# Optimization experiments

Measured on AMD Instinct MI355X. Metric: run time of the kernel, lower is better.

## Reference

```python
import jax, jax.numpy as jnp
import numpy as np

N = 50000      # nodes
E = 800000     # edges (no self loops; module re-adds them)
F_IN = 128     # feats_per_node
H1, C1 = 8, 32     # conv1: heads=8, out=32 -> concat hidden = 256
H2, C2 = 1, 128    # conv2: heads=1, out=128, concat=False (mean)
NEG = 0.2      # leaky relu slope


def _glorot(key, shape):
    fan_in, fan_out = shape[-1], int(np.prod(shape[:-1]))
    lim = float(np.sqrt(6.0 / (fan_in + fan_out)))
    return jax.random.uniform(key, shape, jnp.float32, -lim, lim)


def setup_inputs() -> dict:
    key = jax.random.key(0)
    ks = jax.random.split(key, 10)
    x = jax.random.normal(ks[0], (N, F_IN), jnp.float32)
    src = jax.random.randint(ks[1], (E,), 0, N, dtype=jnp.int32)
    off = jax.random.randint(ks[2], (E,), 1, N, dtype=jnp.int32)
    dst = (src + off) % N  # guarantees src != dst (no self loops)
    edge_index = jnp.stack([src, dst])  # [2, E], row0=source j, row1=target i
    return {
        "x": x,
        "edge_index": edge_index,
        "lin1_w": _glorot(ks[3], (H1 * C1, F_IN)),
        "att1_i": _glorot(ks[4], (1, H1, C1)),
        "att1_j": _glorot(ks[5], (1, H1, C1)),
        "bias1": jnp.zeros((H1 * C1,), jnp.float32),
        "lin2_w": _glorot(ks[6], (C2, H1 * C1)),
        "att2_i": _glorot(ks[7], (1, H2, C2)),
        "att2_j": _glorot(ks[8], (1, H2, C2)),
        "bias2": jnp.zeros((C2,), jnp.float32),
    }


def _gat_conv(x, src, dst, lin_w, att_i, att_j, bias, heads, out_ch, concat):
    n = x.shape[0]
    xh = (x @ lin_w.T).reshape(n, heads, out_ch)          # [n, H, C]
    # add self loops (input edges have none; module removes then adds)
    sl = jnp.arange(n, dtype=src.dtype)
    s = jnp.concatenate([src, sl])
    d = jnp.concatenate([dst, sl])
    # per-node attention logits, then gather per edge (avoids per-edge dot)
    ai = jnp.sum(xh * att_i, axis=-1)                     # [n, H]
    aj = jnp.sum(xh * att_j, axis=-1)                     # [n, H]
    alpha = ai[d] + aj[s]                                 # [Etot, H]
    alpha = jnp.where(alpha > 0, alpha, NEG * alpha)      # leaky relu
    # segment softmax over destination node (every node has a self loop)
    m = jax.ops.segment_max(alpha, d, num_segments=n)
    alpha = jnp.exp(alpha - m[d])
    denom = jax.ops.segment_sum(alpha, d, num_segments=n)
    alpha = alpha / (denom[d] + 1e-16)
    # weighted scatter-add aggregation
    out = jax.ops.segment_sum(xh[s] * alpha[:, :, None], d, num_segments=n)
    out = out.reshape(n, heads * out_ch) if concat else out.mean(axis=1)
    return out + bias


def reference(x, edge_index, lin1_w, att1_i, att1_j, bias1,
              lin2_w, att2_i, att2_j, bias2):
    src, dst = edge_index[0], edge_index[1]
    h = _gat_conv(x, src, dst, lin1_w, att1_i, att1_j, bias1, H1, C1, True)
    h = jax.nn.elu(h)
    return _gat_conv(h, src, dst, lin2_w, att2_i, att2_j, bias2, H2, C2, False)
```

## Files before the change

kernel.cpp:

```cpp
#include <hip/hip_runtime.h>
#include <math.h>

#define NN   50000
#define NE   800000
#define FIN  128
#define HID  256
#define NH1  8
#define C2   128
#define CAP  64
#define NEGS 0.2f

#define NGRP 196
#define CAPB 4608
#define NBIN 782

#define W1R  272
#define W2R  144

#define SWZ(n) ((((n) & 7)) ^ (((n) >> 4) & 7))

typedef __attribute__((ext_vector_type(8))) short bf16x8;
typedef __attribute__((ext_vector_type(4))) float f32x4;

__device__ inline unsigned short f2bf(float f) {
    union { float f; unsigned u; } v; v.f = f;
    unsigned u = v.u;
    u += 0x7fffu + ((u >> 16) & 1u);
    return (unsigned short)(u >> 16);
}
__device__ inline float bf2f(unsigned short h) {
    union { unsigned u; float f; } v; v.u = ((unsigned)h) << 16;
    return v.f;
}

__global__ __launch_bounds__(256) void k_bin(const int* __restrict__ ei,
                                             int* __restrict__ gcnt,
                                             int* __restrict__ gbuf,
                                             const float* __restrict__ w1,
                                             const float* __restrict__ w2,
                                             const float* __restrict__ a1i,
                                             const float* __restrict__ a1j,
                                             const float* __restrict__ a2i,
                                             const float* __restrict__ a2j,
                                             unsigned short* __restrict__ w1e,
                                             unsigned short* __restrict__ w2e) {
    const int B = blockIdx.x, t = threadIdx.x;
    if (B < NBIN) {
        __shared__ int hcnt[NGRP], hbase[NGRP], h2[NGRP];
        for (int k = t; k < NGRP; k += 256) { hcnt[k] = 0; h2[k] = 0; }
        __syncthreads();
        int sv[4], bv[4];
#pragma unroll
        for (int u = 0; u < 4; ++u) {
            const int e = B * 1024 + u * 256 + t;
            if (e < NE) {
                const int s = ei[e], d = ei[NE + e];
                sv[u] = s | ((d & 255) << 16);
                bv[u] = d >> 8;
                atomicAdd(&hcnt[bv[u]], 1);
            } else bv[u] = -1;
        }
        __syncthreads();
        for (int k = t; k < NGRP; k += 256)
            if (hcnt[k]) hbase[k] = atomicAdd(&gcnt[k], hcnt[k]);
        __syncthreads();
#pragma unroll
        for (int u = 0; u < 4; ++u) {
            if (bv[u] >= 0) {
                const int lp = atomicAdd(&h2[bv[u]], 1);
                const int pos = hbase[bv[u]] + lp;
                if (pos < CAPB) gbuf[(size_t)bv[u] * CAPB + pos] = sv[u];
            }
        }
    } else if (B < 1038) {
        const int g = (B - NBIN) * 256 + t;
        if (g < 32768) w1e[g] = f2bf(w1[g]);
        else w2e[g - 32768] = f2bf(w2[g - 32768]);
    } else if (B < 1046) {
        const int g = (B - 1038) * 256 + t;
        const int r = g >> 7, k = g & 127;
        const int h = r & 7;
        const float* att = (r < 8) ? a1i : a1j;
        float s = 0.f;
        for (int c = 0; c < 32; ++c)
            s += att[h * 32 + c] * w1[(h * 32 + c) * FIN + k];
        w1e[(256 + r) * FIN + k] = f2bf(s);
    } else if (B < 1048) {
        const int g = (B - 1046) * 256 + t;
        const int r = g >> 8, k = g & 255;
        const float* att = (r == 0) ? a2i : a2j;
        float s = 0.f;
        for (int c = 0; c < C2; ++c)
            s += att[c] * w2[c * HID + k];
        w2e[(128 + r) * HID + k] = f2bf(s);
    } else {
        const int g = (B - 1048) * 256 + t;
        w2e[130 * HID + g] = 0;
    }
}

__global__ __launch_bounds__(256) void k_build(const int* __restrict__ gcnt,
                                               const int* __restrict__ gbuf,
                                               int* __restrict__ cnt,
                                               int* __restrict__ csr) {
    const int g = blockIdx.x, t = threadIdx.x;
    __shared__ int ccnt[256];
    ccnt[t] = 0;
    __syncthreads();
    const int n = min(gcnt[g], CAPB);
    const int64_t base = (int64_t)g * CAPB;
    for (int k0 = 0; k0 < n; k0 += 1024) {
        int vv[4];
#pragma unroll
        for (int u = 0; u < 4; ++u) {
            const int k = k0 + u * 256 + t;
            vv[u] = (k < n) ? gbuf[base + k] : -1;
        }
#pragma unroll
        for (int u = 0; u < 4; ++u) {
            if (vv[u] >= 0) {
                const int s = vv[u] & 0xffff;
                const int dlow = (vv[u] >> 16) & 0xff;
                const int slot = atomicAdd(&ccnt[dlow], 1);
                if (slot < CAP)
                    csr[((size_t)g * 256 + dlow) * CAP + slot] = s;
            }
        }
    }
    __syncthreads();
    const int node = g * 256 + t;
    if (node < NN) cnt[node] = ccnt[t];
}

__global__ __launch_bounds__(512, 4) void k_gemm1(const float* __restrict__ x,
                                                  const unsigned short* __restrict__ wb,
                                                  unsigned short* __restrict__ xh,
                                                  unsigned char* __restrict__ xq,
                                                  float* __restrict__ scl,
                                                  float* __restrict__ ai,
                                                  float* __restrict__ aj) {
    __shared__ unsigned short wl[W1R * FIN];
    const int t = threadIdx.x;
    for (int idx = t; idx < W1R * 16; idx += 512) {
        const int row = idx >> 4, c = idx & 15;
        *(int4*)((char*)wl + row * 256 + ((c ^ SWZ(row)) << 4)) =
            *(const int4*)(wb + row * FIN + c * 8);
    }
    __syncthreads();

    const int w = t >> 6, l = t & 63, m = l & 15, q = l >> 4;
    const int arow = blockIdx.x * 128 + w * 16 + m;
    const int rowc = arow < NN ? arow : NN - 1;

    f32x4 acc[17];
#pragma unroll
    for (int nt = 0; nt < 17; ++nt)
#pragma unroll
        for (int b = 0; b < 4; ++b) acc[nt][b] = 0.f;

#pragma unroll
    for (int ks = 0; ks < 4; ++ks) {
        const int k0 = ks * 32 + q * 8;
        const float4 a0 = *(const float4*)(x + (size_t)rowc * FIN + k0);
        const float4 a1 = *(const float4*)(x + (size_t)rowc * FIN + k0 + 4);
        bf16x8 af;
        af[0] = (short)f2bf(a0.x); af[1] = (short)f2bf(a0.y);
        af[2] = (short)f2bf(a0.z); af[3] = (short)f2bf(a0.w);
        af[4] = (short)f2bf(a1.x); af[5] = (short)f2bf(a1.y);
        af[6] = (short)f2bf(a1.z); af[7] = (short)f2bf(a1.w);
        const int cb = ks * 4 + q;
#pragma unroll
        for (int nt = 0; nt < 17; ++nt) {
            const int n = (nt < 16) ? (m * 16 + nt) : (256 + m);
            const bf16x8 bf = *(const bf16x8*)((const char*)wl + n * 256 + ((cb ^ SWZ(n)) << 4));
            acc[nt] = __builtin_amdgcn_mfma_f32_16x16x32_bf16(af, bf, acc[nt], 0, 0, 0);
        }
    }

    const int orow = blockIdx.x * 128 + w * 16 + 4 * q;
#pragma unroll
    for (int b = 0; b < 4; ++b) {
        if (orow + b >= NN) break;
        const int row = orow + b;
        float mx = 1e-20f;
#pragma unroll
        for (int nt = 0; nt < 16; ++nt) mx = fmaxf(mx, fabsf(acc[nt][b]));
#pragma unroll
        for (int off = 1; off < 16; off <<= 1) mx = fmaxf(mx, __shfl_xor(mx, off, 16));
        const float qsc = 127.f / mx;
        unsigned bw[8];
#pragma unroll
        for (int k = 0; k < 8; ++k)
            bw[k] = (unsigned)f2bf(acc[2 * k][b]) | ((unsigned)f2bf(acc[2 * k + 1][b]) << 16);
        int4* bd = (int4*)(xh + (size_t)row * HID + m * 16);
        bd[0] = make_int4(bw[0], bw[1], bw[2], bw[3]);
        bd[1] = make_int4(bw[4], bw[5], bw[6], bw[7]);
        unsigned qw[4];
#pragma unroll
        for (int k = 0; k < 4; ++k) {
            const int q0 = (int)rintf(acc[4 * k + 0][b] * qsc) + 128;
            const int q1 = (int)rintf(acc[4 * k + 1][b] * qsc) + 128;
            const int q2 = (int)rintf(acc[4 * k + 2][b] * qsc) + 128;
            const int q3 = (int)rintf(acc[4 * k + 3][b] * qsc) + 128;
            qw[k] = (unsigned)q0 | ((unsigned)q1 << 8) | ((unsigned)q2 << 16) | ((unsigned)q3 << 24);
        }
        *(int4*)(xq + (size_t)row * HID + m * 16) = make_int4(qw[0], qw[1], qw[2], qw[3]);
        if (m == 0) scl[row] = mx * (1.f / 127.f);
        if (m < 8) ai[row * NH1 + m]       = acc[16][b];
        else       aj[row * NH1 + (m - 8)] = acc[16][b];
    }
}

__global__ __launch_bounds__(256) void k_agg1(const unsigned char* __restrict__ xq,
                                              const float* __restrict__ scl,
                                              const unsigned short* __restrict__ xh,
                                              const float* __restrict__ ai,
                                              const float* __restrict__ aj,
                                              const int* __restrict__ cnt,
                                              const int* __restrict__ csr,
                                              const float* __restrict__ bias,
                                              unsigned short* __restrict__ hout) {
    const int lane = threadIdx.x & 63;
    const int i    = blockIdx.x * 4 + (threadIdx.x >> 6);
    const int sub  = lane & 15;
    const int quad = lane >> 4;
    const int myh  = sub >> 1;
    const float a_i = ai[i * NH1 + myh];

    const int deg = min(cnt[i], CAP);
    const int* rowp = csr + (size_t)i * CAP;
    const int svals = (lane < deg) ? rowp[lane] : i;

    float acc[16];
#pragma unroll
    for (int k = 0; k < 16; ++k) acc[k] = 0.f;
    float dsum = 0.f, wsum = 0.f;

    for (int it = 0; it < deg; it += 8) {
#pragma unroll
        for (int u = 0; u < 2; ++u) {
            const int e = it + u * 4 + quad;
            const int s = __shfl(svals, e & 63, 64);
            float aw = a_i + aj[s * NH1 + myh];
            aw = aw > 0.f ? aw : NEGS * aw;
            const float wv = (e < deg) ? __expf(aw) : 0.f;
            dsum += wv;
            const float wvs = wv * scl[s];
            wsum += wvs;
            const int4 raw = ((const int4*)(xq + (size_t)s * HID))[sub];
            const unsigned dx = (unsigned)raw.x, dy = (unsigned)raw.y;
            const unsigned dz = (unsigned)raw.z, dw = (unsigned)raw.w;
            acc[ 0] += wvs * (float)( dx        & 0xffu);
            acc[ 1] += wvs * (float)((dx >>  8) & 0xffu);
            acc[ 2] += wvs * (float)((dx >> 16) & 0xffu);
            acc[ 3] += wvs * (float)( dx >> 24        );
            acc[ 4] += wvs * (float)( dy        & 0xffu);
            acc[ 5] += wvs * (float)((dy >>  8) & 0xffu);
            acc[ 6] += wvs * (float)((dy >> 16) & 0xffu);
            acc[ 7] += wvs * (float)( dy >> 24        );
            acc[ 8] += wvs * (float)( dz        & 0xffu);
            acc[ 9] += wvs * (float)((dz >>  8) & 0xffu);
            acc[10] += wvs * (float)((dz >> 16) & 0xffu);
            acc[11] += wvs * (float)( dz >> 24        );
            acc[12] += wvs * (float)( dw        & 0xffu);
            acc[13] += wvs * (float)((dw >>  8) & 0xffu);
            acc[14] += wvs * (float)((dw >> 16) & 0xffu);
            acc[15] += wvs * (float)( dw >> 24        );
        }
    }
    dsum += __shfl_xor(dsum, 16, 64);
    dsum += __shfl_xor(dsum, 32, 64);
    wsum += __shfl_xor(wsum, 16, 64);
    wsum += __shfl_xor(wsum, 32, 64);
#pragma unroll
    for (int k = 0; k < 16; ++k) {
        acc[k] += __shfl_xor(acc[k], 16, 64);
        acc[k] += __shfl_xor(acc[k], 32, 64);
    }

    float aws = a_i + aj[i * NH1 + myh];
    aws = aws > 0.f ? aws : NEGS * aws;
    const float wself = __expf(aws);
    dsum += wself;
    const ushort4 sv = *(const ushort4*)(xh + (size_t)i * HID + sub * 16 + quad * 4);

    const float inv = 1.f / (dsum + 1e-16f);
    const float c128 = 128.f * wsum;
    const float4 b = ((const float4*)bias)[sub * 4 + quad];
    float4 o;
    o.x = (acc[quad * 4 + 0] - c128 + wself * bf2f(sv.x)) * inv + b.x;
    o.y = (acc[quad * 4 + 1] - c128 + wself * bf2f(sv.y)) * inv + b.y;
    o.z = (acc[quad * 4 + 2] - c128 + wself * bf2f(sv.z)) * inv + b.z;
    o.w = (acc[quad * 4 + 3] - c128 + wself * bf2f(sv.w)) * inv + b.w;
    o.x = o.x > 0.f ? o.x : expm1f(o.x);
    o.y = o.y > 0.f ? o.y : expm1f(o.y);
    o.z = o.z > 0.f ? o.z : expm1f(o.z);
    o.w = o.w > 0.f ? o.w : expm1f(o.w);
    ushort4 ov;
    ov.x = f2bf(o.x); ov.y = f2bf(o.y); ov.z = f2bf(o.z); ov.w = f2bf(o.w);
    ((ushort4*)(hout + (size_t)i * HID))[sub * 4 + quad] = ov;
}

__global__ __launch_bounds__(512, 4) void k_gemm2(const unsigned short* __restrict__ h1,
                                                  const unsigned short* __restrict__ wb,
                                                  unsigned short* __restrict__ xh2,
                                                  unsigned char* __restrict__ xq2,
                                                  float* __restrict__ scl2,
                                                  float* __restrict__ ai2,
                                                  float* __restrict__ aj2) {
    __shared__ unsigned short wl[W2R * HID];
    const int t = threadIdx.x;
    for (int idx = t; idx < W2R * 32; idx += 512) {
        const int row = idx >> 5, c = idx & 31;
        *(int4*)((char*)wl + row * 512 + ((c ^ SWZ(row)) << 4)) =
            *(const int4*)(wb + row * HID + c * 8);
    }
    __syncthreads();

    const int w = t >> 6, l = t & 63, m = l & 15, q = l >> 4;
    const int arow = blockIdx.x * 128 + w * 16 + m;
    const int rowc = arow < NN ? arow : NN - 1;

    f32x4 acc[9];
#pragma unroll
    for (int nt = 0; nt < 9; ++nt)
#pragma unroll
        for (int b = 0; b < 4; ++b) acc[nt][b] = 0.f;

#pragma unroll
    for (int ks = 0; ks < 8; ++ks) {
        const int k0 = ks * 32 + q * 8;
        const bf16x8 af = *(const bf16x8*)(h1 + (size_t)rowc * HID + k0);
        const int cb = ks * 4 + q;
#pragma unroll
        for (int nt = 0; nt < 9; ++nt) {
            const int n = (nt < 8) ? (m * 8 + nt) : (128 + m);
            const bf16x8 bf = *(const bf16x8*)((const char*)wl + n * 512 + ((cb ^ SWZ(n)) << 4));
            acc[nt] = __builtin_amdgcn_mfma_f32_16x16x32_bf16(af, bf, acc[nt], 0, 0, 0);
        }
    }

    const int orow = blockIdx.x * 128 + w * 16 + 4 * q;
#pragma unroll
    for (int b = 0; b < 4; ++b) {
        if (orow + b >= NN) break;
        const int row = orow + b;
        float mx = 1e-20f;
#pragma unroll
        for (int nt = 0; nt < 8; ++nt) mx = fmaxf(mx, fabsf(acc[nt][b]));
#pragma unroll
        for (int off = 1; off < 16; off <<= 1) mx = fmaxf(mx, __shfl_xor(mx, off, 16));
        const float qsc = 127.f / mx;
        unsigned bw[4];
#pragma unroll
        for (int k = 0; k < 4; ++k)
            bw[k] = (unsigned)f2bf(acc[2 * k][b]) | ((unsigned)f2bf(acc[2 * k + 1][b]) << 16);
        *(int4*)(xh2 + (size_t)row * C2 + m * 8) = make_int4(bw[0], bw[1], bw[2], bw[3]);
        unsigned qw[2];
#pragma unroll
        for (int k = 0; k < 2; ++k) {
            const int q0 = (int)rintf(acc[4 * k + 0][b] * qsc) + 128;
            const int q1 = (int)rintf(acc[4 * k + 1][b] * qsc) + 128;
            const int q2 = (int)rintf(acc[4 * k + 2][b] * qsc) + 128;
            const int q3 = (int)rintf(acc[4 * k + 3][b] * qsc) + 128;
            qw[k] = (unsigned)q0 | ((unsigned)q1 << 8) | ((unsigned)q2 << 16) | ((unsigned)q3 << 24);
        }
        *(int2*)(xq2 + (size_t)row * C2 + m * 8) = make_int2(qw[0], qw[1]);
        if (m == 0) scl2[row] = mx * (1.f / 127.f);
        if (m == 0) ai2[row] = acc[8][b];
        if (m == 1) aj2[row] = acc[8][b];
    }
}

__global__ __launch_bounds__(256) void k_agg2(const unsigned char* __restrict__ xq2,
                                              const float* __restrict__ scl2,
                                              const unsigned short* __restrict__ xh2,
                                              const float* __restrict__ ai2v,
                                              const float* __restrict__ aj2v,
                                              const int* __restrict__ cnt,
                                              const int* __restrict__ csr,
                                              const float* __restrict__ bias,
                                              float* __restrict__ out) {
    const int lane = threadIdx.x & 63;
    const int i    = blockIdx.x * 4 + (threadIdx.x >> 6);
    const int sub  = lane & 7;
    const int oct  = lane >> 3;
    const float a_i = ai2v[i];

    const int deg = min(cnt[i], CAP);
    const int* rowp = csr + (size_t)i * CAP;
    const int svals = (lane < deg) ? rowp[lane] : i;

    float acc[16];
#pragma unroll
    for (int k = 0; k < 16; ++k) acc[k] = 0.f;
    float dsum = 0.f, wsum = 0.f;

    for (int it = 0; it < deg; it += 16) {
#pragma unroll
        for (int u = 0; u < 2; ++u) {
            const int e = it + u * 8 + oct;
            const int s = __shfl(svals, e & 63, 64);
            float aw = a_i + aj2v[s];
            aw = aw > 0.f ? aw : NEGS * aw;
            const float wv = (e < deg) ? __expf(aw) : 0.f;
            dsum += wv;
            const float wvs = wv * scl2[s];
            wsum += wvs;
            const int4 raw = ((const int4*)(xq2 + (size_t)s * C2))[sub];
            const unsigned dx = (unsigned)raw.x, dy = (unsigned)raw.y;
            const unsigned dz = (unsigned)raw.z, dw = (unsigned)raw.w;
            acc[ 0] += wvs * (float)( dx        & 0xffu);
            acc[ 1] += wvs * (float)((dx >>  8) & 0xffu);
            acc[ 2] += wvs * (float)((dx >> 16) & 0xffu);
            acc[ 3] += wvs * (float)( dx >> 24        );
            acc[ 4] += wvs * (float)( dy        & 0xffu);
            acc[ 5] += wvs * (float)((dy >>  8) & 0xffu);
            acc[ 6] += wvs * (float)((dy >> 16) & 0xffu);
            acc[ 7] += wvs * (float)( dy >> 24        );
            acc[ 8] += wvs * (float)( dz        & 0xffu);
            acc[ 9] += wvs * (float)((dz >>  8) & 0xffu);
            acc[10] += wvs * (float)((dz >> 16) & 0xffu);
            acc[11] += wvs * (float)( dz >> 24        );
            acc[12] += wvs * (float)( dw        & 0xffu);
            acc[13] += wvs * (float)((dw >>  8) & 0xffu);
            acc[14] += wvs * (float)((dw >> 16) & 0xffu);
            acc[15] += wvs * (float)( dw >> 24        );
        }
    }
    dsum += __shfl_xor(dsum, 8, 64);
    dsum += __shfl_xor(dsum, 16, 64);
    dsum += __shfl_xor(dsum, 32, 64);
    wsum += __shfl_xor(wsum, 8, 64);
    wsum += __shfl_xor(wsum, 16, 64);
    wsum += __shfl_xor(wsum, 32, 64);
#pragma unroll
    for (int k = 0; k < 16; ++k) {
        acc[k] += __shfl_xor(acc[k], 8, 64);
        acc[k] += __shfl_xor(acc[k], 16, 64);
        acc[k] += __shfl_xor(acc[k], 32, 64);
    }

    float aws = a_i + aj2v[i];
    aws = aws > 0.f ? aws : NEGS * aws;
    const float wself = __expf(aws);
    dsum += wself;
    const ushort2 sv = *(const ushort2*)(xh2 + (size_t)i * C2 + sub * 16 + oct * 2);

    const float inv = 1.f / (dsum + 1e-16f);
    const float c128 = 128.f * wsum;
    const float2 b = ((const float2*)bias)[sub * 8 + oct];
    float2 o;
    o.x = (acc[oct * 2 + 0] - c128 + wself * bf2f(sv.x)) * inv + b.x;
    o.y = (acc[oct * 2 + 1] - c128 + wself * bf2f(sv.y)) * inv + b.y;
    ((float2*)(out + (size_t)i * C2))[sub * 8 + oct] = o;
}

extern "C" void kernel_launch(void* const* d_in, const int* in_sizes, int n_in,
                              void* d_out, int out_size, void* d_ws, size_t ws_size,
                              hipStream_t stream) {
    const float* x      = (const float*)d_in[0];
    const int*   ei     = (const int*)  d_in[1];
    const float* lin1_w = (const float*)d_in[2];
    const float* att1_i = (const float*)d_in[3];
    const float* att1_j = (const float*)d_in[4];
    const float* bias1  = (const float*)d_in[5];
    const float* lin2_w = (const float*)d_in[6];
    const float* att2_i = (const float*)d_in[7];
    const float* att2_j = (const float*)d_in[8];
    const float* bias2  = (const float*)d_in[9];
    float* out = (float*)d_out;

    char* wsb = (char*)d_ws;
    size_t off = 0;
    auto alloc = [&](size_t bytes) -> void* {
        void* p = wsb + off;
        off += (bytes + 255) & ~(size_t)255;
        return p;
    };
    int*            gcnt   = (int*)           alloc((size_t)NGRP * 4);
    int*            gbuf   = (int*)           alloc((size_t)NGRP * CAPB * 4);
    int*            cnt    = (int*)           alloc((size_t)NN * 4);
    int*            csr    = (int*)           alloc((size_t)NN * CAP * 4);
    unsigned short* w1e    = (unsigned short*)alloc((size_t)W1R * FIN * 2);
    unsigned short* w2e    = (unsigned short*)alloc((size_t)W2R * HID * 2);
    unsigned short* xh1    = (unsigned short*)alloc((size_t)NN * HID * 2);
    unsigned char*  xq1    = (unsigned char*) alloc((size_t)NN * HID);
    float*          scl1   = (float*)         alloc((size_t)NN * 4);
    float*          ai1    = (float*)         alloc((size_t)NN * NH1 * 4);
    float*          aj1    = (float*)         alloc((size_t)NN * NH1 * 4);
    unsigned short* h1     = (unsigned short*)alloc((size_t)NN * HID * 2);
    unsigned short* xh2    = (unsigned short*)alloc((size_t)NN * C2 * 2);
    unsigned char*  xq2    = (unsigned char*) alloc((size_t)NN * C2);
    float*          scl2   = (float*)         alloc((size_t)NN * 4);
    float*          ai2    = (float*)         alloc((size_t)NN * 4);
    float*          aj2    = (float*)         alloc((size_t)NN * 4);
    if (off > ws_size) return;

    const int gm = (NN + 127) / 128;
    hipMemsetAsync(gcnt, 0, (size_t)NGRP * 4, stream);
    k_bin<<<1062, 256, 0, stream>>>(ei, gcnt, gbuf, lin1_w, lin2_w,
                                    att1_i, att1_j, att2_i, att2_j, w1e, w2e);
    k_build<<<NGRP, 256, 0, stream>>>(gcnt, gbuf, cnt, csr);
    k_gemm1<<<gm, 512, 0, stream>>>(x, w1e, xh1, xq1, scl1, ai1, aj1);
    k_agg1<<<NN / 4, 256, 0, stream>>>(xq1, scl1, xh1, ai1, aj1, cnt, csr, bias1, h1);
    k_gemm2<<<gm, 512, 0, stream>>>(h1, w2e, xh2, xq2, scl2, ai2, aj2);
    k_agg2<<<NN / 4, 256, 0, stream>>>(xq2, scl2, xh2, ai2, aj2, cnt, csr, bias2, out);
}
```

Before: 154.9 us.

## Merge CSR build into gemm1 launch and pack agg1 accumulators as float2

```diff
diff --git a/kernel.cpp b/kernel.cpp
--- a/kernel.cpp
+++ b/kernel.cpp
@@ -21,6 +21,7 @@
 
 typedef __attribute__((ext_vector_type(8))) short bf16x8;
 typedef __attribute__((ext_vector_type(4))) float f32x4;
+typedef __attribute__((ext_vector_type(2))) float f32x2;
 
 __device__ inline unsigned short f2bf(float f) {
     union { float f; unsigned u; } v; v.f = f;
@@ -99,48 +100,54 @@
     }
 }
 
-__global__ __launch_bounds__(256) void k_build(const int* __restrict__ gcnt,
-                                               const int* __restrict__ gbuf,
-                                               int* __restrict__ cnt,
-                                               int* __restrict__ csr) {
-    const int g = blockIdx.x, t = threadIdx.x;
-    __shared__ int ccnt[256];
-    ccnt[t] = 0;
-    __syncthreads();
-    const int n = min(gcnt[g], CAPB);
-    const int64_t base = (int64_t)g * CAPB;
-    for (int k0 = 0; k0 < n; k0 += 1024) {
-        int vv[4];
-#pragma unroll
-        for (int u = 0; u < 4; ++u) {
-            const int k = k0 + u * 256 + t;
-            vv[u] = (k < n) ? gbuf[base + k] : -1;
-        }
-#pragma unroll
-        for (int u = 0; u < 4; ++u) {
-            if (vv[u] >= 0) {
-                const int s = vv[u] & 0xffff;
-                const int dlow = (vv[u] >> 16) & 0xff;
-                const int slot = atomicAdd(&ccnt[dlow], 1);
-                if (slot < CAP)
-                    csr[((size_t)g * 256 + dlow) * CAP + slot] = s;
-            }
-        }
-    }
-    __syncthreads();
-    const int node = g * 256 + t;
-    if (node < NN) cnt[node] = ccnt[t];
-}
-
-__global__ __launch_bounds__(512, 4) void k_gemm1(const float* __restrict__ x,
+__global__ __launch_bounds__(512, 2) void k_gemm1(const float* __restrict__ x,
                                                   const unsigned short* __restrict__ wb,
+                                                  const int* __restrict__ gcnt,
+                                                  const int* __restrict__ gbuf,
+                                                  int* __restrict__ cnt,
+                                                  int* __restrict__ csr,
                                                   unsigned short* __restrict__ xh,
                                                   unsigned char* __restrict__ xq,
                                                   float* __restrict__ scl,
                                                   float* __restrict__ ai,
                                                   float* __restrict__ aj) {
     __shared__ unsigned short wl[W1R * FIN];
+    __shared__ int ccnt[256];
     const int t = threadIdx.x;
+
+    if (blockIdx.x < NGRP) {
+        const int g = blockIdx.x;
+        if (t < 256) ccnt[t] = 0;
+        __syncthreads();
+        const int n = min(gcnt[g], CAPB);
+        const int64_t base = (int64_t)g * CAPB;
+        for (int k0 = 0; k0 < n; k0 += 2048) {
+            int vv[4];
+#pragma unroll
+            for (int u = 0; u < 4; ++u) {
+                const int k = k0 + u * 512 + t;
+                vv[u] = (k < n) ? gbuf[base + k] : -1;
+            }
+#pragma unroll
+            for (int u = 0; u < 4; ++u) {
+                if (vv[u] >= 0) {
+                    const int s = vv[u] & 0xffff;
+                    const int dlow = (vv[u] >> 16) & 0xff;
+                    const int slot = atomicAdd(&ccnt[dlow], 1);
+                    if (slot < CAP)
+                        csr[((size_t)g * 256 + dlow) * CAP + slot] = s;
+                }
+            }
+        }
+        __syncthreads();
+        if (t < 256) {
+            const int node = g * 256 + t;
+            if (node < NN) cnt[node] = ccnt[t];
+        }
+        return;
+    }
+
+    const int bid = blockIdx.x - NGRP;
     for (int idx = t; idx < W1R * 16; idx += 512) {
         const int row = idx >> 4, c = idx & 15;
         *(int4*)((char*)wl + row * 256 + ((c ^ SWZ(row)) << 4)) =
@@ -149,7 +156,7 @@
     __syncthreads();
 
     const int w = t >> 6, l = t & 63, m = l & 15, q = l >> 4;
-    const int arow = blockIdx.x * 128 + w * 16 + m;
+    const int arow = bid * 128 + w * 16 + m;
     const int rowc = arow < NN ? arow : NN - 1;
 
     f32x4 acc[17];
@@ -177,7 +184,7 @@
         }
     }
 
-    const int orow = blockIdx.x * 128 + w * 16 + 4 * q;
+    const int orow = bid * 128 + w * 16 + 4 * q;
 #pragma unroll
     for (int b = 0; b < 4; ++b) {
         if (orow + b >= NN) break;
@@ -231,9 +238,9 @@
     const int* rowp = csr + (size_t)i * CAP;
     const int svals = (lane < deg) ? rowp[lane] : i;
 
-    float acc[16];
-#pragma unroll
-    for (int k = 0; k < 16; ++k) acc[k] = 0.f;
+    f32x2 acc2[8];
+#pragma unroll
+    for (int k = 0; k < 8; ++k) acc2[k] = (f32x2){0.f, 0.f};
     float dsum = 0.f, wsum = 0.f;
 
     for (int it = 0; it < deg; it += 8) {
@@ -247,35 +254,32 @@
             dsum += wv;
             const float wvs = wv * scl[s];
             wsum += wvs;
+            const f32x2 pv = {wvs, wvs};
             const int4 raw = ((const int4*)(xq + (size_t)s * HID))[sub];
             const unsigned dx = (unsigned)raw.x, dy = (unsigned)raw.y;
             const unsigned dz = (unsigned)raw.z, dw = (unsigned)raw.w;
-            acc[ 0] += wvs * (float)( dx        & 0xffu);
-            acc[ 1] += wvs * (float)((dx >>  8) & 0xffu);
-            acc[ 2] += wvs * (float)((dx >> 16) & 0xffu);
-            acc[ 3] += wvs * (float)( dx >> 24        );
-            acc[ 4] += wvs * (float)( dy        & 0xffu);
-            acc[ 5] += wvs * (float)((dy >>  8) & 0xffu);
-            acc[ 6] += wvs * (float)((dy >> 16) & 0xffu);
-            acc[ 7] += wvs * (float)( dy >> 24        );
-            acc[ 8] += wvs * (float)( dz        & 0xffu);
-            acc[ 9] += wvs * (float)((dz >>  8) & 0xffu);
-            acc[10] += wvs * (float)((dz >> 16) & 0xffu);
-            acc[11] += wvs * (float)( dz >> 24        );
-            acc[12] += wvs * (float)( dw        & 0xffu);
-            acc[13] += wvs * (float)((dw >>  8) & 0xffu);
-            acc[14] += wvs * (float)((dw >> 16) & 0xffu);
-            acc[15] += wvs * (float)( dw >> 24        );
+            f32x2 d;
+            d = (f32x2){(float)( dx        & 0xffu), (float)((dx >>  8) & 0xffu)}; acc2[0] += pv * d;
+            d = (f32x2){(float)((dx >> 16) & 0xffu), (float)( dx >> 24        )}; acc2[1] += pv * d;
+            d = (f32x2){(float)( dy        & 0xffu), (float)((dy >>  8) & 0xffu)}; acc2[2] += pv * d;
+            d = (f32x2){(float)((dy >> 16) & 0xffu), (float)( dy >> 24        )}; acc2[3] += pv * d;
+            d = (f32x2){(float)( dz        & 0xffu), (float)((dz >>  8) & 0xffu)}; acc2[4] += pv * d;
+            d = (f32x2){(float)((dz >> 16) & 0xffu), (float)( dz >> 24        )}; acc2[5] += pv * d;
+            d = (f32x2){(float)( dw        & 0xffu), (float)((dw >>  8) & 0xffu)}; acc2[6] += pv * d;
+            d = (f32x2){(float)((dw >> 16) & 0xffu), (float)( dw >> 24        )}; acc2[7] += pv * d;
         }
     }
     dsum += __shfl_xor(dsum, 16, 64);
     dsum += __shfl_xor(dsum, 32, 64);
     wsum += __shfl_xor(wsum, 16, 64);
     wsum += __shfl_xor(wsum, 32, 64);
-#pragma unroll
-    for (int k = 0; k < 16; ++k) {
-        acc[k] += __shfl_xor(acc[k], 16, 64);
-        acc[k] += __shfl_xor(acc[k], 32, 64);
+    float accf[16];
+#pragma unroll
+    for (int k = 0; k < 8; ++k) {
+        float x0 = acc2[k].x, x1 = acc2[k].y;
+        x0 += __shfl_xor(x0, 16, 64); x0 += __shfl_xor(x0, 32, 64);
+        x1 += __shfl_xor(x1, 16, 64); x1 += __shfl_xor(x1, 32, 64);
+        accf[2 * k] = x0; accf[2 * k + 1] = x1;
     }
 
     float aws = a_i + aj[i * NH1 + myh];
@@ -288,10 +292,10 @@
     const float c128 = 128.f * wsum;
     const float4 b = ((const float4*)bias)[sub * 4 + quad];
     float4 o;
-    o.x = (acc[quad * 4 + 0] - c128 + wself * bf2f(sv.x)) * inv + b.x;
-    o.y = (acc[quad * 4 + 1] - c128 + wself * bf2f(sv.y)) * inv + b.y;
-    o.z = (acc[quad * 4 + 2] - c128 + wself * bf2f(sv.z)) * inv + b.z;
-    o.w = (acc[quad * 4 + 3] - c128 + wself * bf2f(sv.w)) * inv + b.w;
+    o.x = (accf[quad * 4 + 0] - c128 + wself * bf2f(sv.x)) * inv + b.x;
+    o.y = (accf[quad * 4 + 1] - c128 + wself * bf2f(sv.y)) * inv + b.y;
+    o.z = (accf[quad * 4 + 2] - c128 + wself * bf2f(sv.z)) * inv + b.z;
+    o.w = (accf[quad * 4 + 3] - c128 + wself * bf2f(sv.w)) * inv + b.w;
     o.x = o.x > 0.f ? o.x : expm1f(o.x);
     o.y = o.y > 0.f ? o.y : expm1f(o.y);
     o.z = o.z > 0.f ? o.z : expm1f(o.z);
@@ -501,8 +505,8 @@
     hipMemsetAsync(gcnt, 0, (size_t)NGRP * 4, stream);
     k_bin<<<1062, 256, 0, stream>>>(ei, gcnt, gbuf, lin1_w, lin2_w,
                                     att1_i, att1_j, att2_i, att2_j, w1e, w2e);
-    k_build<<<NGRP, 256, 0, stream>>>(gcnt, gbuf, cnt, csr);
-    k_gemm1<<<gm, 512, 0, stream>>>(x, w1e, xh1, xq1, scl1, ai1, aj1);
+    k_gemm1<<<NGRP + gm, 512, 0, stream>>>(x, w1e, gcnt, gbuf, cnt, csr,
+                                           xh1, xq1, scl1, ai1, aj1);
     k_agg1<<<NN / 4, 256, 0, stream>>>(xq1, scl1, xh1, ai1, aj1, cnt, csr, bias1, h1);
     k_gemm2<<<gm, 512, 0, stream>>>(h1, w2e, xh2, xq2, scl2, ai2, aj2);
     k_agg2<<<NN / 4, 256, 0, stream>>>(xq2, scl2, xh2, ai2, aj2, cnt, csr, bias2, out);
```

Measured after the change: 150.2 us, median of 2. -3.0%, faster.
